# Optimization experiments

Measured on AMD Instinct MI355X. Metric: run time of the kernel, lower is better.

Reference implementation:

```python
import jax, jax.numpy as jnp
import numpy as np

NUM_HEADS = 12
HEAD_DIM = 64  # dim=768 // 12
SCALE = HEAD_DIM ** (-0.5)  # NOTE: original divides q by this -> multiplies by sqrt(head_dim)


def setup_inputs() -> dict:
    key = jax.random.key(0)
    k1, k2, k3 = jax.random.split(key, 3)
    B, N, C = 1, 4096, 768
    x = jax.random.normal(k1, (B, N, C), dtype=jnp.float32)
    qkv_w = jax.random.normal(k2, (3 * C, C), dtype=jnp.float32) * 0.01
    qkv_b = jnp.zeros((3 * C,), dtype=jnp.float32)
    proj_w = jax.random.normal(k3, (C, C), dtype=jnp.float32) * 0.01
    proj_b = jnp.zeros((C,), dtype=jnp.float32)
    return {"x": x, "qkv_w": qkv_w, "qkv_b": qkv_b, "proj_w": proj_w, "proj_b": proj_b}


def reference(x, qkv_w, qkv_b, proj_w, proj_b):
    B, N, C = x.shape
    H, D = NUM_HEADS, HEAD_DIM
    # qkv projection: [B,N,3C]
    qkv = x @ qkv_w.T + qkv_b
    qkv = qkv.reshape(B, N, 3, H, D).transpose(2, 0, 3, 1, 4)  # [3,B,H,N,D]
    q, k, v = qkv[0], qkv[1], qkv[2]
    # Faithful quirk: q / scale with scale = D**-0.5 => logits scaled by sqrt(D)
    attn = jnp.einsum('bhnd,bhmd->bhnm', q / SCALE, k)  # [B,H,N,N]
    attn = jax.nn.softmax(attn, axis=-1)
    # dropout omitted (eval mode / deterministic reference)
    out = jnp.einsum('bhnm,bhmd->bhnd', attn, v)  # [B,H,N,D]
    out = out.transpose(0, 2, 1, 3).reshape(B, N, C)
    out = out @ proj_w.T + proj_b
    return out
```

## Files before the change

kernel.cpp:

```cpp
#include <hip/hip_runtime.h>


typedef short bf16x8 __attribute__((ext_vector_type(8)));
typedef float f32x4 __attribute__((ext_vector_type(4)));
typedef unsigned short u16;
typedef unsigned int u32;

__device__ __forceinline__ u16 f2bf(float f) {
  u32 u = __float_as_uint(f);
  u = (u + 0x7fffu + ((u >> 16) & 1u)) >> 16;
  return (u16)u;
}

__device__ __forceinline__ u32 cvtpk(float a, float b) {
  u32 r;
  asm("v_cvt_pk_bf16_f32 %0, %1, %2" : "=v"(r) : "v"(a), "v"(b));
  return r;
}

__device__ __forceinline__ void gload16(const void* g, void* l) {
  __builtin_amdgcn_global_load_lds(
      (const __attribute__((address_space(1))) unsigned int*)g,
      (__attribute__((address_space(3))) unsigned int*)l, 16, 0, 0);
}

__device__ __forceinline__ void pl32swap(u32& x, u32& y) {
  asm("v_permlane32_swap_b32 %0, %1" : "+v"(x), "+v"(y));
}
__device__ __forceinline__ void pl16swap(u32& x, u32& y) {
  asm("v_permlane16_swap_b32 %0, %1" : "+v"(x), "+v"(y));
}

__global__ void cast3(const float* __restrict__ a, int na4,
                      const float* __restrict__ b, int nb4,
                      const float* __restrict__ c, int nc4,
                      u16* __restrict__ oa, u16* __restrict__ obp, u16* __restrict__ oc) {
  int i = blockIdx.x * blockDim.x + threadIdx.x;
  const float* src;
  u16* dst;
  int j = i;
  if (i < na4) { src = a; dst = oa; }
  else if (i < na4 + nb4) { src = b; dst = obp; j = i - na4; }
  else if (i < na4 + nb4 + nc4) { src = c; dst = oc; j = i - na4 - nb4; }
  else return;
  float4 v = ((const float4*)src)[j];
  ushort4 o;
  o.x = f2bf(v.x); o.y = f2bf(v.y); o.z = f2bf(v.z); o.w = f2bf(v.w);
  ((ushort4*)dst)[j] = o;
}

template <int MODE>
__global__ __launch_bounds__(256, 2) void gemm_bt(
    const u16* __restrict__ A, const u16* __restrict__ B,
    const float* __restrict__ bias,
    u16* __restrict__ qb, u16* __restrict__ kbuf, u16* __restrict__ vb,
    float* __restrict__ outp, int K, int N) {
  __shared__ __align__(16) u16 As[128 * 32];
  __shared__ __align__(16) u16 Bs[128 * 32];
  const int tid = threadIdx.x, lane = tid & 63, w = tid >> 6;
  const int wr = w >> 1, wc = w & 1, quad = lane >> 4, l15 = lane & 15;
  const int m0 = blockIdx.y * 128, n0 = blockIdx.x * 128;

  f32x4 acc[4][4];
#pragma unroll
  for (int i = 0; i < 4; ++i)
#pragma unroll
    for (int j = 0; j < 4; ++j) acc[i][j] = (f32x4){0.f, 0.f, 0.f, 0.f};

  for (int k0 = 0; k0 < K; k0 += 32) {
    __syncthreads();
#pragma unroll
    for (int i = 0; i < 2; ++i) {
      int chunk = i * 256 + w * 64 + lane;
      int row = chunk >> 2, kc = chunk & 3;
      gload16(A + (size_t)(m0 + row) * K + k0 + kc * 8, (char*)As + chunk * 16);
      gload16(B + (size_t)(n0 + row) * K + k0 + kc * 8, (char*)Bs + chunk * 16);
    }
    __syncthreads();
    bf16x8 af[4], bfr[4];
#pragma unroll
    for (int mi = 0; mi < 4; ++mi)
      af[mi] = *(const bf16x8*)&As[(wr * 64 + mi * 16 + l15) * 32 + quad * 8];
#pragma unroll
    for (int ni = 0; ni < 4; ++ni)
      bfr[ni] = *(const bf16x8*)&Bs[(wc * 64 + ni * 16 + l15) * 32 + quad * 8];
#pragma unroll
    for (int mi = 0; mi < 4; ++mi)
#pragma unroll
      for (int ni = 0; ni < 4; ++ni)
        acc[mi][ni] = __builtin_amdgcn_mfma_f32_16x16x32_bf16(af[mi], bfr[ni], acc[mi][ni], 0, 0, 0);
  }

#pragma unroll
  for (int mi = 0; mi < 4; ++mi) {
    int row = m0 + wr * 64 + mi * 16 + quad * 4;
#pragma unroll
    for (int ni = 0; ni < 4; ++ni) {
      int col = n0 + wc * 64 + ni * 16 + l15;
      float bv = bias[col];
      if (MODE == 0) {
        int t = col / 768;
        int rem = col - t * 768;
        int hh = rem >> 6, d = rem & 63;
        if (t == 2) {
          u16* dst = vb + (size_t)hh * 64 * 4096 + (size_t)d * 4096 + row;
          ushort4 pk;
          pk.x = f2bf(acc[mi][ni][0] + bv);
          pk.y = f2bf(acc[mi][ni][1] + bv);
          pk.z = f2bf(acc[mi][ni][2] + bv);
          pk.w = f2bf(acc[mi][ni][3] + bv);
          *(ushort4*)dst = pk;
        } else {
          u16* dst = (t == 0 ? qb : kbuf) + (size_t)hh * 4096 * 64 + d;
          float sc = (t == 0) ? 11.541560327111707f : 1.f;
#pragma unroll
          for (int r = 0; r < 4; ++r)
            dst[(size_t)(row + r) * 64] = f2bf((acc[mi][ni][r] + bv) * sc);
        }
      } else {
#pragma unroll
        for (int r = 0; r < 4; ++r)
          outp[(size_t)(row + r) * N + col] = acc[mi][ni][r] + bv;
      }
    }
  }
}

__global__ __launch_bounds__(256, 3) void flash_attn(
    const u16* __restrict__ qb, const u16* __restrict__ kb,
    const u16* __restrict__ vtg, u16* __restrict__ ob) {
  __shared__ __align__(16) u16 Ks[2][64 * 64];
  __shared__ __align__(16) u16 Vs[2][64 * 64];

  const int b = blockIdx.x;
  const int g = (b & 7) * 96 + (b >> 3);
  const int h = g >> 6;
  const int q0 = (g & 63) * 64;

  const int tid = threadIdx.x, lane = tid & 63, w = tid >> 6;
  const int quad = lane >> 4, l15 = lane & 15;
  const int qh2 = w >> 1, kh = w & 1;
  const u16* qptr = qb + (size_t)h * 4096 * 64;
  const u16* kptr = kb + (size_t)h * 4096 * 64;
  const u16* vptr = vtg + (size_t)h * 64 * 4096;
  const int sw = l15 & 7;
  const int u0 = (quad ^ sw) * 8;
  const int u1 = ((quad + 4) ^ sw) * 8;
  const int uv = (((kh << 2) + quad) ^ sw) * 8;

  int c0 = w * 64 + lane, c1 = 256 + w * 64 + lane;
  int r0s = c0 >> 3, j0s = ((c0 & 7) ^ (r0s & 7)) * 8;
  int r1s = c1 >> 3, j1s = ((c1 & 7) ^ (r1s & 7)) * 8;

  bf16x8 qf[2][2];
#pragma unroll
  for (int qt = 0; qt < 2; ++qt)
#pragma unroll
    for (int c = 0; c < 2; ++c)
      qf[qt][c] = *(const bf16x8*)&qptr[(size_t)(q0 + qh2 * 32 + qt * 16 + l15) * 64 + c * 32 + quad * 8];

  f32x4 oacc[2][4];
#pragma unroll
  for (int qt = 0; qt < 2; ++qt)
#pragma unroll
    for (int dt = 0; dt < 4; ++dt) oacc[qt][dt] = (f32x4){0.f, 0.f, 0.f, 0.f};
  float lsum[2] = {0.f, 0.f};
  const f32x4 zero4 = (f32x4){0.f, 0.f, 0.f, 0.f};

  bf16x8 pfprev[2], vprev[4];

  gload16(kptr + (size_t)r0s * 64 + j0s, (char*)&Ks[0][0] + c0 * 16);
  gload16(kptr + (size_t)r1s * 64 + j1s, (char*)&Ks[0][0] + c1 * 16);
  gload16(vptr + (size_t)r0s * 4096 + j0s, (char*)&Vs[0][0] + c0 * 16);
  gload16(vptr + (size_t)r1s * 4096 + j1s, (char*)&Vs[0][0] + c1 * 16);

  for (int t = 0; t < 64; ++t) {
    const int buf = t & 1;
    __syncthreads();
    if (t < 63) {
      int kt1 = (t + 1) * 64;
      gload16(kptr + (size_t)(kt1 + r0s) * 64 + j0s, (char*)&Ks[buf ^ 1][0] + c0 * 16);
      gload16(kptr + (size_t)(kt1 + r1s) * 64 + j1s, (char*)&Ks[buf ^ 1][0] + c1 * 16);
      gload16(vptr + (size_t)r0s * 4096 + kt1 + j0s, (char*)&Vs[buf ^ 1][0] + c0 * 16);
      gload16(vptr + (size_t)r1s * 4096 + kt1 + j1s, (char*)&Vs[buf ^ 1][0] + c1 * 16);
    }

    bf16x8 kf[2][2];
#pragma unroll
    for (int mt = 0; mt < 2; ++mt) {
      const u16* kr = &Ks[buf][((kh << 5) + mt * 16 + l15) * 64];
      kf[mt][0] = *(const bf16x8*)(kr + u0);
      kf[mt][1] = *(const bf16x8*)(kr + u1);
    }

    __builtin_amdgcn_s_setprio(1);
    if (t > 0) {
#pragma unroll
      for (int qt = 0; qt < 2; ++qt)
#pragma unroll
        for (int dt = 0; dt < 4; ++dt)
          oacc[qt][dt] = __builtin_amdgcn_mfma_f32_16x16x32_bf16(pfprev[qt], vprev[dt], oacc[qt][dt], 0, 0, 0);
    }

    f32x4 st[2][2];
#pragma unroll
    for (int mt = 0; mt < 2; ++mt)
#pragma unroll
      for (int qt = 0; qt < 2; ++qt) {
        f32x4 z = __builtin_amdgcn_mfma_f32_16x16x32_bf16(kf[mt][0], qf[qt][0], zero4, 0, 0, 0);
        st[mt][qt] = __builtin_amdgcn_mfma_f32_16x16x32_bf16(kf[mt][1], qf[qt][1], z, 0, 0, 0);
      }
    __builtin_amdgcn_s_setprio(0);

#pragma unroll
    for (int dt = 0; dt < 4; ++dt)
      vprev[dt] = *(const bf16x8*)(&Vs[buf][(dt * 16 + l15) * 64] + uv);

#pragma unroll
    for (int qt = 0; qt < 2; ++qt) {
      float p00 = __builtin_amdgcn_exp2f(st[0][qt][0]);
      float p01 = __builtin_amdgcn_exp2f(st[0][qt][1]);
      float p02 = __builtin_amdgcn_exp2f(st[0][qt][2]);
      float p03 = __builtin_amdgcn_exp2f(st[0][qt][3]);
      float p10 = __builtin_amdgcn_exp2f(st[1][qt][0]);
      float p11 = __builtin_amdgcn_exp2f(st[1][qt][1]);
      float p12 = __builtin_amdgcn_exp2f(st[1][qt][2]);
      float p13 = __builtin_amdgcn_exp2f(st[1][qt][3]);
      lsum[qt] += ((p00 + p01) + (p02 + p03)) + ((p10 + p11) + (p12 + p13));
      u32 x0 = cvtpk(p00, p01), x1 = cvtpk(p02, p03);
      u32 y0 = cvtpk(p10, p11), y1 = cvtpk(p12, p13);
      pl32swap(x0, y0); pl16swap(x0, y0);
      pl32swap(x1, y1); pl16swap(x1, y1);
      union { u32 u[4]; bf16x8 v; } pu;
      pu.u[0] = x0; pu.u[1] = x1; pu.u[2] = y0; pu.u[3] = y1;
      pfprev[qt] = pu.v;
    }
  }

#pragma unroll
  for (int qt = 0; qt < 2; ++qt)
#pragma unroll
    for (int dt = 0; dt < 4; ++dt)
      oacc[qt][dt] = __builtin_amdgcn_mfma_f32_16x16x32_bf16(pfprev[qt], vprev[dt], oacc[qt][dt], 0, 0, 0);

  __syncthreads();
#pragma unroll
  for (int qt = 0; qt < 2; ++qt) {
    lsum[qt] += __shfl_xor(lsum[qt], 16);
    lsum[qt] += __shfl_xor(lsum[qt], 32);
  }
  float* ored = (float*)&Ks[0][0];
  float* lred = (float*)&Vs[0][0];
  if (kh == 1) {
#pragma unroll
    for (int qt = 0; qt < 2; ++qt) {
#pragma unroll
      for (int dt = 0; dt < 4; ++dt)
        *(f32x4*)&ored[((((qh2 * 2 + qt) * 4 + dt) * 64) + lane) * 4] = oacc[qt][dt];
      if (quad == 0) lred[(qh2 * 2 + qt) * 16 + l15] = lsum[qt];
    }
  }
  __syncthreads();
  if (kh == 0) {
#pragma unroll
    for (int qt = 0; qt < 2; ++qt) {
      float linv = 1.f / (lsum[qt] + lred[(qh2 * 2 + qt) * 16 + l15]);
      float r0 = __shfl(linv, quad * 4 + 0);
      float r1 = __shfl(linv, quad * 4 + 1);
      float r2 = __shfl(linv, quad * 4 + 2);
      float r3 = __shfl(linv, quad * 4 + 3);
#pragma unroll
      for (int dt = 0; dt < 4; ++dt) {
        f32x4 oo = *(const f32x4*)&ored[((((qh2 * 2 + qt) * 4 + dt) * 64) + lane) * 4];
        int row = q0 + qh2 * 32 + qt * 16 + quad * 4;
        u16* op = ob + (size_t)row * 768 + h * 64 + dt * 16 + l15;
        op[0]       = f2bf((oacc[qt][dt][0] + oo[0]) * r0);
        op[768]     = f2bf((oacc[qt][dt][1] + oo[1]) * r1);
        op[2 * 768] = f2bf((oacc[qt][dt][2] + oo[2]) * r2);
        op[3 * 768] = f2bf((oacc[qt][dt][3] + oo[3]) * r3);
      }
    }
  }
}

extern "C" void kernel_launch(void* const* d_in, const int* in_sizes, int n_in,
                              void* d_out, int out_size, void* d_ws, size_t ws_size,
                              hipStream_t stream) {
  const float* x      = (const float*)d_in[0];
  const float* qkv_w  = (const float*)d_in[1];
  const float* qkv_b  = (const float*)d_in[2];
  const float* proj_w = (const float*)d_in[3];
  const float* proj_b = (const float*)d_in[4];
  float* out = (float*)d_out;

  const int N = 4096, C = 768, H = 12, D = 64, C3 = 2304;
  char* ws = (char*)d_ws;
  size_t off = 0;
  u16* xb    = (u16*)(ws + off); off += (size_t)N * C * 2;
  u16* wqkv  = (u16*)(ws + off); off += (size_t)C3 * C * 2;
  u16* wproj = (u16*)(ws + off); off += (size_t)C * C * 2;
  u16* qbuf  = (u16*)(ws + off); off += (size_t)H * N * D * 2;
  u16* kbuf  = (u16*)(ws + off); off += (size_t)H * N * D * 2;
  u16* vbuf  = (u16*)(ws + off); off += (size_t)H * N * D * 2;
  u16* aob = xb;

  const int na4 = N * C / 4, nb4 = C3 * C / 4, nc4 = C * C / 4;
  int ntot = na4 + nb4 + nc4;
  cast3<<<(ntot + 255) / 256, 256, 0, stream>>>(x, na4, qkv_w, nb4, proj_w, nc4, xb, wqkv, wproj);

  dim3 g1(C3 / 128, N / 128);
  gemm_bt<0><<<g1, 256, 0, stream>>>(xb, wqkv, qkv_b, qbuf, kbuf, vbuf, nullptr, C, C3);

  flash_attn<<<768, 256, 0, stream>>>(qbuf, kbuf, vbuf, aob);

  dim3 g3(C / 128, N / 128);
  gemm_bt<1><<<g3, 256, 0, stream>>>(aob, wproj, proj_b, nullptr, nullptr, nullptr, out, C, C);
}
```

Before: 124.5 us.

## Compute softmax row sums via MFMA with ones, unroll attention loop, shrink proj GEMM tile

The flash attention kernel now gets row sums of P from an extra MFMA against a vector of bf16 ones, replacing the per-iteration scalar adds and the final cross-lane shuffles. The key/value loop is unrolled by two with a lambda and pointer increments, so double-buffer indices are constant and address math is lighter. The output projection GEMM uses 64-row tiles to launch twice as many blocks and fill more compute units. The MFMA sum uses the bf16-rounded probabilities, which keeps it consistent with the PV numerator but adds matrix-unit work in the hot loop.

```diff
diff --git a/kernel.cpp b/kernel.cpp
--- a/kernel.cpp
+++ b/kernel.cpp
@@ -55,45 +55,52 @@
     const float* __restrict__ bias,
     u16* __restrict__ qb, u16* __restrict__ kbuf, u16* __restrict__ vb,
     float* __restrict__ outp, int K, int N) {
-  __shared__ __align__(16) u16 As[128 * 32];
+  constexpr int TM = (MODE == 1) ? 64 : 128;
+  constexpr int MI = TM / 32;
+  __shared__ __align__(16) u16 As[TM * 32];
   __shared__ __align__(16) u16 Bs[128 * 32];
   const int tid = threadIdx.x, lane = tid & 63, w = tid >> 6;
   const int wr = w >> 1, wc = w & 1, quad = lane >> 4, l15 = lane & 15;
-  const int m0 = blockIdx.y * 128, n0 = blockIdx.x * 128;
-
-  f32x4 acc[4][4];
-#pragma unroll
-  for (int i = 0; i < 4; ++i)
+  const int m0 = blockIdx.y * TM, n0 = blockIdx.x * 128;
+
+  f32x4 acc[MI][4];
+#pragma unroll
+  for (int i = 0; i < MI; ++i)
 #pragma unroll
     for (int j = 0; j < 4; ++j) acc[i][j] = (f32x4){0.f, 0.f, 0.f, 0.f};
 
   for (int k0 = 0; k0 < K; k0 += 32) {
     __syncthreads();
 #pragma unroll
-    for (int i = 0; i < 2; ++i) {
-      int chunk = i * 256 + w * 64 + lane;
+    for (int i = 0; i < TM / 64; ++i) {
+      int chunk = i * 256 + tid;
       int row = chunk >> 2, kc = chunk & 3;
       gload16(A + (size_t)(m0 + row) * K + k0 + kc * 8, (char*)As + chunk * 16);
+    }
+#pragma unroll
+    for (int i = 0; i < 2; ++i) {
+      int chunk = i * 256 + tid;
+      int row = chunk >> 2, kc = chunk & 3;
       gload16(B + (size_t)(n0 + row) * K + k0 + kc * 8, (char*)Bs + chunk * 16);
     }
     __syncthreads();
-    bf16x8 af[4], bfr[4];
-#pragma unroll
-    for (int mi = 0; mi < 4; ++mi)
-      af[mi] = *(const bf16x8*)&As[(wr * 64 + mi * 16 + l15) * 32 + quad * 8];
+    bf16x8 af[MI], bfr[4];
+#pragma unroll
+    for (int mi = 0; mi < MI; ++mi)
+      af[mi] = *(const bf16x8*)&As[(wr * (TM / 2) + mi * 16 + l15) * 32 + quad * 8];
 #pragma unroll
     for (int ni = 0; ni < 4; ++ni)
       bfr[ni] = *(const bf16x8*)&Bs[(wc * 64 + ni * 16 + l15) * 32 + quad * 8];
 #pragma unroll
-    for (int mi = 0; mi < 4; ++mi)
+    for (int mi = 0; mi < MI; ++mi)
 #pragma unroll
       for (int ni = 0; ni < 4; ++ni)
         acc[mi][ni] = __builtin_amdgcn_mfma_f32_16x16x32_bf16(af[mi], bfr[ni], acc[mi][ni], 0, 0, 0);
   }
 
 #pragma unroll
-  for (int mi = 0; mi < 4; ++mi) {
-    int row = m0 + wr * 64 + mi * 16 + quad * 4;
+  for (int mi = 0; mi < MI; ++mi) {
+    int row = m0 + wr * (TM / 2) + mi * 16 + quad * 4;
 #pragma unroll
     for (int ni = 0; ni < 4; ++ni) {
       int col = n0 + wc * 64 + ni * 16 + l15;
@@ -160,12 +167,17 @@
       qf[qt][c] = *(const bf16x8*)&qptr[(size_t)(q0 + qh2 * 32 + qt * 16 + l15) * 64 + c * 32 + quad * 8];
 
   f32x4 oacc[2][4];
-#pragma unroll
-  for (int qt = 0; qt < 2; ++qt)
+  f32x4 lacc[2];
+#pragma unroll
+  for (int qt = 0; qt < 2; ++qt) {
+    lacc[qt] = (f32x4){0.f, 0.f, 0.f, 0.f};
 #pragma unroll
     for (int dt = 0; dt < 4; ++dt) oacc[qt][dt] = (f32x4){0.f, 0.f, 0.f, 0.f};
-  float lsum[2] = {0.f, 0.f};
+  }
   const f32x4 zero4 = (f32x4){0.f, 0.f, 0.f, 0.f};
+  bf16x8 onesf;
+#pragma unroll
+  for (int i = 0; i < 8; ++i) onesf[i] = (short)0x3F80;
 
   bf16x8 pfprev[2], vprev[4];
 
@@ -174,15 +186,19 @@
   gload16(vptr + (size_t)r0s * 4096 + j0s, (char*)&Vs[0][0] + c0 * 16);
   gload16(vptr + (size_t)r1s * 4096 + j1s, (char*)&Vs[0][0] + c1 * 16);
 
-  for (int t = 0; t < 64; ++t) {
-    const int buf = t & 1;
+  const u16* ks0 = kptr + (size_t)(64 + r0s) * 64 + j0s;
+  const u16* ks1 = kptr + (size_t)(64 + r1s) * 64 + j1s;
+  const u16* vs0 = vptr + (size_t)r0s * 4096 + 64 + j0s;
+  const u16* vs1 = vptr + (size_t)r1s * 4096 + 64 + j1s;
+
+  auto body = [&](int t, int buf) {
     __syncthreads();
     if (t < 63) {
-      int kt1 = (t + 1) * 64;
-      gload16(kptr + (size_t)(kt1 + r0s) * 64 + j0s, (char*)&Ks[buf ^ 1][0] + c0 * 16);
-      gload16(kptr + (size_t)(kt1 + r1s) * 64 + j1s, (char*)&Ks[buf ^ 1][0] + c1 * 16);
-      gload16(vptr + (size_t)r0s * 4096 + kt1 + j0s, (char*)&Vs[buf ^ 1][0] + c0 * 16);
-      gload16(vptr + (size_t)r1s * 4096 + kt1 + j1s, (char*)&Vs[buf ^ 1][0] + c1 * 16);
+      gload16(ks0, (char*)&Ks[buf ^ 1][0] + c0 * 16);
+      gload16(ks1, (char*)&Ks[buf ^ 1][0] + c1 * 16);
+      gload16(vs0, (char*)&Vs[buf ^ 1][0] + c0 * 16);
+      gload16(vs1, (char*)&Vs[buf ^ 1][0] + c1 * 16);
+      ks0 += 64 * 64; ks1 += 64 * 64; vs0 += 64; vs1 += 64;
     }
 
     bf16x8 kf[2][2];
@@ -196,10 +212,12 @@
     __builtin_amdgcn_s_setprio(1);
     if (t > 0) {
 #pragma unroll
-      for (int qt = 0; qt < 2; ++qt)
+      for (int qt = 0; qt < 2; ++qt) {
 #pragma unroll
         for (int dt = 0; dt < 4; ++dt)
           oacc[qt][dt] = __builtin_amdgcn_mfma_f32_16x16x32_bf16(pfprev[qt], vprev[dt], oacc[qt][dt], 0, 0, 0);
+        lacc[qt] = __builtin_amdgcn_mfma_f32_16x16x32_bf16(pfprev[qt], onesf, lacc[qt], 0, 0, 0);
+      }
     }
 
     f32x4 st[2][2];
@@ -226,7 +244,6 @@
       float p11 = __builtin_amdgcn_exp2f(st[1][qt][1]);
       float p12 = __builtin_amdgcn_exp2f(st[1][qt][2]);
       float p13 = __builtin_amdgcn_exp2f(st[1][qt][3]);
-      lsum[qt] += ((p00 + p01) + (p02 + p03)) + ((p10 + p11) + (p12 + p13));
       u32 x0 = cvtpk(p00, p01), x1 = cvtpk(p02, p03);
       u32 y0 = cvtpk(p10, p11), y1 = cvtpk(p12, p13);
       pl32swap(x0, y0); pl16swap(x0, y0);
@@ -235,20 +252,22 @@
       pu.u[0] = x0; pu.u[1] = x1; pu.u[2] = y0; pu.u[3] = y1;
       pfprev[qt] = pu.v;
     }
-  }
-
-#pragma unroll
-  for (int qt = 0; qt < 2; ++qt)
+  };
+
+  for (int tt = 0; tt < 32; ++tt) {
+    body(2 * tt, 0);
+    body(2 * tt + 1, 1);
+  }
+
+#pragma unroll
+  for (int qt = 0; qt < 2; ++qt) {
 #pragma unroll
     for (int dt = 0; dt < 4; ++dt)
       oacc[qt][dt] = __builtin_amdgcn_mfma_f32_16x16x32_bf16(pfprev[qt], vprev[dt], oacc[qt][dt], 0, 0, 0);
+    lacc[qt] = __builtin_amdgcn_mfma_f32_16x16x32_bf16(pfprev[qt], onesf, lacc[qt], 0, 0, 0);
+  }
 
   __syncthreads();
-#pragma unroll
-  for (int qt = 0; qt < 2; ++qt) {
-    lsum[qt] += __shfl_xor(lsum[qt], 16);
-    lsum[qt] += __shfl_xor(lsum[qt], 32);
-  }
   float* ored = (float*)&Ks[0][0];
   float* lred = (float*)&Vs[0][0];
   if (kh == 1) {
@@ -257,27 +276,30 @@
 #pragma unroll
       for (int dt = 0; dt < 4; ++dt)
         *(f32x4*)&ored[((((qh2 * 2 + qt) * 4 + dt) * 64) + lane) * 4] = oacc[qt][dt];
-      if (quad == 0) lred[(qh2 * 2 + qt) * 16 + l15] = lsum[qt];
+      if (l15 == 0) {
+#pragma unroll
+        for (int r = 0; r < 4; ++r)
+          lred[(qh2 * 2 + qt) * 16 + quad * 4 + r] = lacc[qt][r];
+      }
     }
   }
   __syncthreads();
   if (kh == 0) {
 #pragma unroll
     for (int qt = 0; qt < 2; ++qt) {
-      float linv = 1.f / (lsum[qt] + lred[(qh2 * 2 + qt) * 16 + l15]);
-      float r0 = __shfl(linv, quad * 4 + 0);
-      float r1 = __shfl(linv, quad * 4 + 1);
-      float r2 = __shfl(linv, quad * 4 + 2);
-      float r3 = __shfl(linv, quad * 4 + 3);
+      f32x4 linv;
+#pragma unroll
+      for (int r = 0; r < 4; ++r)
+        linv[r] = 1.f / (lacc[qt][r] + lred[(qh2 * 2 + qt) * 16 + quad * 4 + r]);
 #pragma unroll
       for (int dt = 0; dt < 4; ++dt) {
         f32x4 oo = *(const f32x4*)&ored[((((qh2 * 2 + qt) * 4 + dt) * 64) + lane) * 4];
         int row = q0 + qh2 * 32 + qt * 16 + quad * 4;
         u16* op = ob + (size_t)row * 768 + h * 64 + dt * 16 + l15;
-        op[0]       = f2bf((oacc[qt][dt][0] + oo[0]) * r0);
-        op[768]     = f2bf((oacc[qt][dt][1] + oo[1]) * r1);
-        op[2 * 768] = f2bf((oacc[qt][dt][2] + oo[2]) * r2);
-        op[3 * 768] = f2bf((oacc[qt][dt][3] + oo[3]) * r3);
+        op[0]       = f2bf((oacc[qt][dt][0] + oo[0]) * linv[0]);
+        op[768]     = f2bf((oacc[qt][dt][1] + oo[1]) * linv[1]);
+        op[2 * 768] = f2bf((oacc[qt][dt][2] + oo[2]) * linv[2]);
+        op[3 * 768] = f2bf((oacc[qt][dt][3] + oo[3]) * linv[3]);
       }
     }
   }
@@ -313,6 +335,6 @@
 
   flash_attn<<<768, 256, 0, stream>>>(qbuf, kbuf, vbuf, aob);
 
-  dim3 g3(C / 128, N / 128);
+  dim3 g3(C / 128, N / 64);
   gemm_bt<1><<<g3, 256, 0, stream>>>(aob, wproj, proj_b, nullptr, nullptr, nullptr, out, C, C);
 }
```

Measured after the change: 117.4 us, median of 3. 5.7% less time.
